# Performance work log

Measured on AMD Instinct MI355X. Metric: run time of the kernel, lower is better.

Reference implementation:

```python
import jax, jax.numpy as jnp
import numpy as np

B, N, D = 4, 2048, 1024
WIN, K, ALPHA = 4, 8, 0.3


def setup_inputs() -> dict:
    key = jax.random.key(0)
    ks = jax.random.split(key, 16)
    s_d = 1.0 / np.sqrt(D)
    s_2d = 1.0 / np.sqrt(2 * D)
    inp = {
        'mu': jax.random.normal(ks[0], (B, N, D), jnp.float32),
        'pheromone': jax.random.uniform(ks[1], (B, N), jnp.float32),
        'Wq': jax.random.normal(ks[2], (D, D), jnp.float32) * s_d,
        'bq': jnp.zeros((D,), jnp.float32),
        'Wk': jax.random.normal(ks[3], (D, D), jnp.float32) * s_d,
        'bk': jnp.zeros((D,), jnp.float32),
        'Wv': jax.random.normal(ks[4], (D, D), jnp.float32) * s_d,
        'bv': jnp.zeros((D,), jnp.float32),
        'Wm1': jax.random.normal(ks[5], (2 * D, D), jnp.float32) * s_2d,
        'bm1': jnp.zeros((D,), jnp.float32),
        'Wm2': jax.random.normal(ks[6], (D, D), jnp.float32) * s_d,
        'bm2': jnp.zeros((D,), jnp.float32),
        'Wo': jax.random.normal(ks[7], (2 * D, D), jnp.float32) * s_2d,
        'bo': jnp.zeros((D,), jnp.float32),
    }
    return inp


def reference(mu, pheromone, Wq, bq, Wk, bk, Wv, bv, Wm1, bm1, Wm2, bm2, Wo, bo):
    # ---- local windowed gather-MLP ----
    padded = jnp.pad(mu, ((0, 0), (WIN, 0), (0, 0)))  # causal left-pad
    neighbors = jnp.stack([padded[:, WIN - w:WIN - w + N, :] for w in range(1, WIN + 1)], axis=2)
    self_exp = jnp.broadcast_to(mu[:, :, None, :], neighbors.shape)
    cat = jnp.concatenate([self_exp, neighbors], axis=-1)
    h = jax.nn.silu(cat @ Wm1 + bm1) @ Wm2 + bm2
    local_msgs = h.mean(axis=2)  # (B,N,D)

    # ---- causal top-k attention with pheromone bias ----
    q = mu @ Wq + bq
    k = mu @ Wk + bk
    v = mu @ Wv + bv
    scale = 1.0 / jnp.sqrt(jnp.asarray(D, mu.dtype))
    scores = jnp.einsum('bnd,bmd->bnm', q, k) * scale  # (B,N,N)
    scores = scores + ALPHA * pheromone[:, None, :]
    row = jnp.arange(N)
    causal = jnp.where(row[None, :] > row[:, None], -jnp.inf, 0.0).astype(mu.dtype)
    scores = scores + causal[None]
    # top-k sparsification (N > K): softmax over the k kept scores, zeros elsewhere
    vals, idx = jax.lax.top_k(scores, K)  # (B,N,K)
    probs = jax.nn.softmax(vals, axis=-1)
    bi = jnp.arange(B)[:, None, None]
    ni = jnp.arange(N)[None, :, None]
    attn = jnp.zeros_like(scores).at[bi, ni, idx].set(probs)
    global_msgs = jnp.einsum('bnm,bmd->bnd', attn, v)

    return jnp.concatenate([local_msgs, global_msgs], axis=-1) @ Wo + bo
```

## Files before the change

### kernel.cpp

```cpp
#include <hip/hip_runtime.h>
#include <hip/hip_bf16.h>
#include <math.h>

#define B_ 4
#define N_ 2048
#define D_ 1024
#define WIN_ 4
#define KTOP 8
#define ALPHA_ 0.3f
#define SCALE_ (1.0f/32.0f)
#define NCH 16
#define INV2048 0.00048828125f

typedef unsigned short ushortT;
typedef _Float16 halfT;
typedef __attribute__((ext_vector_type(8))) _Float16 half8v;
typedef __attribute__((ext_vector_type(4))) float f32x4;

__device__ inline ushortT h2u(halfT h){ union{halfT h; ushortT u;} x; x.h=h; return x.u; }
__device__ inline halfT  u2h(ushortT u){ union{halfT h; ushortT u;} x; x.u=u; return x.h; }
__device__ inline float  uh2f(ushortT u){ return (float)u2h(u); }

__device__ __forceinline__ void gll16(const ushortT* g, ushortT* l) {
    __builtin_amdgcn_global_load_lds(
        (const __attribute__((address_space(1))) void*)g,
        (__attribute__((address_space(3))) void*)l, 16, 0, 0);
}

__global__ __launch_bounds__(256)
void prep_all(const float* __restrict__ mu, const float* __restrict__ Wm1,
              const float* __restrict__ Wm2, const float* __restrict__ Wv,
              const float* __restrict__ Wo, const float* __restrict__ Wq,
              const float* __restrict__ Wk,
              ushortT* __restrict__ mu_a, ushortT* __restrict__ mu_B,
              ushortT* __restrict__ WtF, ushortT* __restrict__ Wt_m2,
              ushortT* __restrict__ Wt_v, ushortT* __restrict__ Wt_o,
              ushortT* __restrict__ WqT_a, ushortT* __restrict__ WqT_B,
              ushortT* __restrict__ WkT_a, ushortT* __restrict__ WkT_B)
{
    const int bid = blockIdx.x;
    if (bid < 8192) {
        size_t base = ((size_t)bid * 256 + threadIdx.x) * 4;
        float4 v = *reinterpret_cast<const float4*>(&mu[base]);
        float vv[4] = {v.x, v.y, v.z, v.w};
        ushort4 pa, pb;
#pragma unroll
        for (int j = 0; j < 4; ++j) {
            float f = vv[j];
            halfT a = (halfT)f;  float r = f - (float)a;
            halfT b = (halfT)(r * 2048.0f);
            ((ushortT*)&pa)[j] = h2u(a); ((ushortT*)&pb)[j] = h2u(b);
        }
        *reinterpret_cast<ushort4*>(&mu_a[base]) = pa;
        *reinterpret_cast<ushort4*>(&mu_B[base]) = pb;
        return;
    }
    __shared__ float t[32][33];
    int b = bid - 8192;
    const float* W; ushortT* Pa; ushortT* Pb = nullptr;
    int K, lb, split = 0;
    if (b < 1024)      { W = Wm1;                       Pa = WtF;                     K = 1024; lb = b; }
    else if (b < 2048) { W = Wm1 + (size_t)1024 * 1024; Pa = WtF + (size_t)1024*1024; K = 1024; lb = b - 1024; }
    else if (b < 3072) { W = Wm2;  Pa = Wt_m2; K = 1024; lb = b - 2048; }
    else if (b < 4096) { W = Wv;   Pa = Wt_v;  K = 1024; lb = b - 3072; }
    else if (b < 6144) { W = Wo;   Pa = Wt_o;  K = 2048; lb = b - 4096; }
    else if (b < 7168) { W = Wq;   Pa = WqT_a; Pb = WqT_B; K = 1024; lb = b - 6144; split = 1; }
    else               { W = Wk;   Pa = WkT_a; Pb = WkT_B; K = 1024; lb = b - 7168; split = 1; }
    const int Nn = 1024;
    const int k0 = (K == 2048) ? (lb & 63) * 32 : (lb & 31) * 32;
    const int n0 = (K == 2048) ? (lb >> 6) * 32 : (lb >> 5) * 32;
    const int tx = threadIdx.x & 31, ty8 = threadIdx.x >> 5;
#pragma unroll
    for (int p = 0; p < 4; ++p) {
        int kk = p * 8 + ty8;
        t[kk][tx] = W[(size_t)(k0 + kk) * Nn + n0 + tx];
    }
    __syncthreads();
#pragma unroll
    for (int p = 0; p < 4; ++p) {
        int nn = p * 8 + ty8;
        float f = t[tx][nn];
        size_t o = (size_t)(n0 + nn) * K + k0 + tx;
        if (split) {
            halfT a = (halfT)f;  float r = f - (float)a;
            halfT bb = (halfT)(r * 2048.0f);
            Pa[o] = h2u(a); Pb[o] = h2u(bb);
        } else {
            Pa[o] = h2u((halfT)f);
        }
    }
}

__device__ __forceinline__ void gemm_core_h(
    const ushortT* __restrict__ A, int lda, const ushortT* __restrict__ Bt, int ldb,
    const float* __restrict__ bias, void* __restrict__ Cout, int ldc, int K,
    int m0, int n0, int outHalf, ushortT* AsL, ushortT* BsL)
{
    const int tid = threadIdx.x;
    const int w = tid >> 6, lane = tid & 63;
    const int wr = w >> 1, wc = w & 1;

    f32x4 acc[4][4];
#pragma unroll
    for (int mi = 0; mi < 4; ++mi)
#pragma unroll
        for (int ni = 0; ni < 4; ++ni) acc[mi][ni] = (f32x4){0.f, 0.f, 0.f, 0.f};

    for (int k0 = 0; k0 < K; k0 += 64) {
#pragma unroll
        for (int it = 0; it < 4; ++it) {
            int idx = tid + it * 256;
            int row = idx >> 3, c = idx & 7;
            int4 va = *reinterpret_cast<const int4*>(&A[(size_t)(m0 + row) * lda + k0 + c * 8]);
            *reinterpret_cast<int4*>(&AsL[row * 72 + c * 8]) = va;
            int4 vb = *reinterpret_cast<const int4*>(&Bt[(size_t)(n0 + row) * ldb + k0 + c * 8]);
            *reinterpret_cast<int4*>(&BsL[row * 72 + c * 8]) = vb;
        }
        __syncthreads();
#pragma unroll
        for (int kh = 0; kh < 2; ++kh) {
            const int ko = kh * 32 + (lane >> 4) * 8;
            const int rr = lane & 15;
            half8v af[4], bf[4];
#pragma unroll
            for (int mi = 0; mi < 4; ++mi)
                af[mi] = *reinterpret_cast<const half8v*>(&AsL[(wr * 64 + mi * 16 + rr) * 72 + ko]);
#pragma unroll
            for (int ni = 0; ni < 4; ++ni)
                bf[ni] = *reinterpret_cast<const half8v*>(&BsL[(wc * 64 + ni * 16 + rr) * 72 + ko]);
#pragma unroll
            for (int mi = 0; mi < 4; ++mi)
#pragma unroll
                for (int ni = 0; ni < 4; ++ni)
                    acc[mi][ni] = __builtin_amdgcn_mfma_f32_16x16x32_f16(
                        af[mi], bf[ni], acc[mi][ni], 0, 0, 0);
        }
        __syncthreads();
    }

    const int r4 = (lane >> 4) * 4, cl = lane & 15;
#pragma unroll
    for (int mi = 0; mi < 4; ++mi)
#pragma unroll
        for (int ni = 0; ni < 4; ++ni) {
            int row = m0 + wr * 64 + mi * 16 + r4;
            int col = n0 + wc * 64 + ni * 16 + cl;
            float bb = bias ? bias[col] : 0.f;
#pragma unroll
            for (int r = 0; r < 4; ++r) {
                float v = acc[mi][ni][r] + bb;
                if (outHalf)
                    ((ushortT*)Cout)[(size_t)(row + r) * ldc + col] = h2u((halfT)v);
                else
                    ((float*)Cout)[(size_t)(row + r) * ldc + col] = v;
            }
        }
}

template<int OUT_HALF>
__global__ __launch_bounds__(256)
void mfma_gemm_h(const ushortT* __restrict__ A, int lda,
                 const ushortT* __restrict__ Bt, int ldb,
                 const float* __restrict__ bias,
                 void* __restrict__ Cout, int ldc, int K)
{
    __shared__ ushortT AsL[128 * 72];
    __shared__ ushortT BsL[128 * 72];
    gemm_core_h(A, lda, Bt, ldb, bias, Cout, ldc, K,
                blockIdx.y * 128, blockIdx.x * 128, OUT_HALF, AsL, BsL);
}

__global__ __launch_bounds__(256)
void gemm_pf_v(const ushortT* __restrict__ mu_a,
               const ushortT* __restrict__ WtF, const ushortT* __restrict__ Wt_v,
               const float* __restrict__ bv,
               float* __restrict__ PF, ushortT* __restrict__ Vb16)
{
    __shared__ ushortT AsL[128 * 72];
    __shared__ ushortT BsL[128 * 72];
    const int bid = blockIdx.x;
    if (bid < 1024) {
        gemm_core_h(mu_a, D_, WtF, D_, (const float*)nullptr, (void*)PF, 2 * D_, D_,
                    (bid >> 4) * 128, (bid & 15) * 128, 0, AsL, BsL);
    } else {
        const int b2 = bid - 1024;
        gemm_core_h(mu_a, D_, Wt_v, D_, bv, (void*)Vb16, D_, D_,
                    (b2 >> 3) * 128, (b2 & 7) * 128, 1, AsL, BsL);
    }
}

__global__ __launch_bounds__(256)
void silu_mean(const float* __restrict__ P, const float* __restrict__ bm1,
               ushortT* __restrict__ Sb)
{
    size_t idx4 = (size_t)blockIdx.x * blockDim.x + threadIdx.x;
    size_t base = idx4 << 2;
    int row = (int)(base >> 10);
    int col = (int)(base & 1023);
    int n = row & (N_ - 1);
    float4 a = *reinterpret_cast<const float4*>(&P[(size_t)row * 2048 + col]);
    float4 bb = *reinterpret_cast<const float4*>(&bm1[col]);
    a.x += bb.x; a.y += bb.y; a.z += bb.z; a.w += bb.w;
    float sx = 0.f, sy = 0.f, sz = 0.f, sw = 0.f;
#pragma unroll
    for (int w = 1; w <= WIN_; ++w) {
        float xx = a.x, xy = a.y, xz = a.z, xw = a.w;
        if (n >= w) {
            const float4 nb = *reinterpret_cast<const float4*>(
                &P[(size_t)(row - w) * 2048 + 1024 + col]);
            xx += nb.x; xy += nb.y; xz += nb.z; xw += nb.w;
        }
        sx += xx / (1.f + __expf(-xx));
        sy += xy / (1.f + __expf(-xy));
        sz += xz / (1.f + __expf(-xz));
        sw += xw / (1.f + __expf(-xw));
    }
    ushort4 o = {h2u((halfT)(sx * 0.25f)), h2u((halfT)(sy * 0.25f)),
                 h2u((halfT)(sz * 0.25f)), h2u((halfT)(sw * 0.25f))};
    *reinterpret_cast<ushort4*>(&Sb[base]) = o;
}

__device__ inline void topk_insert(float (&tv)[KTOP], int (&ti)[KTOP], float s, int m)
{
    if ((s > tv[KTOP-1]) || (s == tv[KTOP-1] && m < ti[KTOP-1])) {
        float cs = s; int ci = m;
#pragma unroll
        for (int q = 0; q < KTOP; ++q) {
            bool beats = (cs > tv[q]) || (cs == tv[q] && ci < ti[q]);
            if (beats) { float t0 = tv[q]; int t1 = ti[q];
                         tv[q] = cs; ti[q] = ci; cs = t0; ci = t1; }
        }
    }
}

#define SPLIT3H_COMPUTE(Tb, wr, wc, lane, acc0, acc1)                           \
    {                                                                           \
        const int rr_ = (lane) & 15, q_ = (lane) >> 4;                          \
        const int Rb0_ = (wc) * 32 + rr_;                                       \
        const int Rb1_ = Rb0_ + 16;                                             \
        half8v ba0_ = *reinterpret_cast<const half8v*>(                         \
            &Tb[2 * 4096 + Rb0_ * 32 + ((q_ ^ ((Rb0_ >> 1) & 3)) << 3)]);       \
        half8v ba1_ = *reinterpret_cast<const half8v*>(                         \
            &Tb[2 * 4096 + Rb1_ * 32 + ((q_ ^ ((Rb1_ >> 1) & 3)) << 3)]);       \
        half8v bB0_ = *reinterpret_cast<const half8v*>(                         \
            &Tb[3 * 4096 + Rb0_ * 32 + ((q_ ^ ((Rb0_ >> 1) & 3)) << 3)]);       \
        half8v bB1_ = *reinterpret_cast<const half8v*>(                         \
            &Tb[3 * 4096 + Rb1_ * 32 + ((q_ ^ ((Rb1_ >> 1) & 3)) << 3)]);       \
        _Pragma("unroll")                                                       \
        for (int mi_ = 0; mi_ < 4; ++mi_) {                                     \
            const int Ra_ = (wr) * 64 + mi_ * 16 + rr_;                         \
            const int sw_ = (q_ ^ ((Ra_ >> 1) & 3)) << 3;                       \
            half8v aA_ = *reinterpret_cast<const half8v*>(&Tb[Ra_ * 32 + sw_]); \
            acc0[mi_][0] = __builtin_amdgcn_mfma_f32_16x16x32_f16(              \
                aA_, ba0_, acc0[mi_][0], 0, 0, 0);                              \
            acc0[mi_][1] = __builtin_amdgcn_mfma_f32_16x16x32_f16(              \
                aA_, ba1_, acc0[mi_][1], 0, 0, 0);                              \
            acc1[mi_][0] = __builtin_amdgcn_mfma_f32_16x16x32_f16(              \
                aA_, bB0_, acc1[mi_][0], 0, 0, 0);                              \
            acc1[mi_][1] = __builtin_amdgcn_mfma_f32_16x16x32_f16(              \
                aA_, bB1_, acc1[mi_][1], 0, 0, 0);                              \
        }                                                                       \
        _Pragma("unroll")                                                       \
        for (int mi_ = 0; mi_ < 4; ++mi_) {                                     \
            const int Ra_ = (wr) * 64 + mi_ * 16 + rr_;                         \
            const int sw_ = (q_ ^ ((Ra_ >> 1) & 3)) << 3;                       \
            half8v aB_ = *reinterpret_cast<const half8v*>(                      \
                &Tb[4096 + Ra_ * 32 + sw_]);                                    \
            acc1[mi_][0] = __builtin_amdgcn_mfma_f32_16x16x32_f16(              \
                aB_, ba0_, acc1[mi_][0], 0, 0, 0);                              \
            acc1[mi_][1] = __builtin_amdgcn_mfma_f32_16x16x32_f16(              \
                aB_, ba1_, acc1[mi_][1], 0, 0, 0);                              \
        }                                                                       \
    }

#define STAGE4(lb, koff)                                                        \
    {                                                                           \
        gll16(gp + goff + (koff), lb);                                          \
        gll16(gp + goff + (koff) + 16 * D_, (lb) + 512);                        \
        gll16(gp + goff + (koff) + 32 * D_, (lb) + 1024);                       \
        gll16(gp + goff + (koff) + 48 * D_, (lb) + 1536);                       \
    }

__global__ __launch_bounds__(512, 2)
void qk_proj(const ushortT* __restrict__ A0, const ushortT* __restrict__ A1,
             const ushortT* __restrict__ QWa, const ushortT* __restrict__ QWB,
             const ushortT* __restrict__ KWa, const ushortT* __restrict__ KWB,
             const float* __restrict__ bq, const float* __restrict__ bk,
             ushortT* __restrict__ Qa, ushortT* __restrict__ QB,
             ushortT* __restrict__ Ka, ushortT* __restrict__ KB)
{
    __shared__ ushortT TT[16384];

    const int half = blockIdx.x >> 9;
    int lin = blockIdx.x & 511;
    lin = (lin & 7) * 64 + (lin >> 3);
    const int m0 = (lin >> 3) * 128;
    const int n0 = (lin & 7) * 128;

    const ushortT* B0 = half ? KWa : QWa;
    const ushortT* B1 = half ? KWB : QWB;
    const float* bias = half ? bk : bq;
    ushortT* Pa = half ? Ka : Qa;
    ushortT* Pb = half ? KB : QB;

    const int tid = threadIdx.x;
    const int wid = tid >> 6, lane = tid & 63;
    const int wr = wid >> 2, wc = wid & 3;

    const int pl = wid >> 1;
    const int hb = (wid & 1) * 64;
    const ushortT* gp = (pl == 0) ? A0 : (pl == 1) ? A1 : (pl == 2) ? B0 : B1;
    const int rbase = (pl < 2 ? m0 : n0) + hb + (lane >> 2);
    const int cg8 = ((lane & 3) ^ ((lane >> 3) & 3)) << 3;
    const size_t goff = (size_t)rbase * D_ + cg8;
    ushortT* lb0 = &TT[pl * 4096 + hb * 32];

    f32x4 acc0[4][2], acc1[4][2];
#pragma unroll
    for (int mi = 0; mi < 4; ++mi) {
        acc0[mi][0] = (f32x4){0,0,0,0}; acc0[mi][1] = (f32x4){0,0,0,0};
        acc1[mi][0] = (f32x4){0,0,0,0}; acc1[mi][1] = (f32x4){0,0,0,0};
    }

    for (int ks = 0; ks < 32; ++ks) {
        STAGE4(lb0, (size_t)ks * 32)
        __syncthreads();
        __builtin_amdgcn_s_setprio(1);
        SPLIT3H_COMPUTE(TT, wr, wc, lane, acc0, acc1)
        __builtin_amdgcn_s_setprio(0);
        __syncthreads();
    }

    const int r4 = (lane >> 4) * 4, cl = lane & 15;
#pragma unroll
    for (int mi = 0; mi < 4; ++mi)
#pragma unroll
        for (int ni = 0; ni < 2; ++ni) {
            int col = n0 + wc * 32 + ni * 16 + cl;
            float bb = bias[col];
#pragma unroll
            for (int r = 0; r < 4; ++r) {
                int row = m0 + wr * 64 + mi * 16 + r4 + r;
                float v = acc0[mi][ni][r] + INV2048 * acc1[mi][ni][r] + bb;
                halfT a = (halfT)v;  float r1 = v - (float)a;
                halfT b = (halfT)(r1 * 2048.0f);
                size_t o = (size_t)row * D_ + col;
                Pa[o] = h2u(a); Pb[o] = h2u(b);
            }
        }
}

__global__ __launch_bounds__(512, 2)
void attn_scores_h(const ushortT* __restrict__ Qa, const ushortT* __restrict__ QB,
                   const ushortT* __restrict__ Ka, const ushortT* __restrict__ KB,
                   const float* __restrict__ pher,
                   float* __restrict__ WV, int* __restrict__ WI)
{
    __shared__ ushortT TT[16384];
    __shared__ float Ps[128];
    __shared__ float PV[32 * 4 * 8];
    __shared__ int   PI[32 * 4 * 8];
    float* MV = reinterpret_cast<float*>(&TT[0]);
    int*   MI = reinterpret_cast<int*>((char*)&TT[0] + 16384);

    int lin = blockIdx.y * 136 + blockIdx.x;
    lin = (lin & 7) * 68 + (lin >> 3);
    const int b = lin / 136;
    const int xy = lin - b * 136;
    int g = 0;
    while ((g + 1) * (g + 2) / 2 <= xy) ++g;
    const int ch = xy - g * (g + 1) / 2;
    const int n0 = g * 128;
    const int m0 = ch * 128;
    const size_t bN = (size_t)b * N_;

    const int tid = threadIdx.x;
    const int wid = tid >> 6, lane = tid & 63;
    const int wr = wid >> 2, wc = wid & 3;

    if (tid < 128) Ps[tid] = pher[bN + m0 + tid];

    const int pl = wid >> 1;
    const int hb = (wid & 1) * 64;
    const ushortT* gp = (pl == 0) ? Qa : (pl == 1) ? QB : (pl == 2) ? Ka : KB;
    const size_t rbase = bN + (pl < 2 ? n0 : m0) + hb + (lane >> 2);
    const int cg8 = ((lane & 3) ^ ((lane >> 3) & 3)) << 3;
    const size_t goff = rbase * (size_t)D_ + cg8;
    ushortT* lb0 = &TT[pl * 4096 + hb * 32];

    f32x4 acc0[4][2], acc1[4][2];
#pragma unroll
    for (int mi = 0; mi < 4; ++mi) {
        acc0[mi][0] = (f32x4){0,0,0,0}; acc0[mi][1] = (f32x4){0,0,0,0};
        acc1[mi][0] = (f32x4){0,0,0,0}; acc1[mi][1] = (f32x4){0,0,0,0};
    }

    for (int ks = 0; ks < 32; ++ks) {
        STAGE4(lb0, (size_t)ks * 32)
        __syncthreads();
        __builtin_amdgcn_s_setprio(1);
        SPLIT3H_COMPUTE(TT, wr, wc, lane, acc0, acc1)
        __builtin_amdgcn_s_setprio(0);
        __syncthreads();
    }

    const int r4 = (lane >> 4) * 4, cl = lane & 15;
    for (int p = 0; p < 4; ++p) {
        __syncthreads();
        if (wr == (p >> 1)) {
#pragma unroll
            for (int mi2 = 0; mi2 < 2; ++mi2) {
                const int mi = (p & 1) * 2 + mi2;
#pragma unroll
                for (int ni = 0; ni < 2; ++ni) {
                    int col = wc * 32 + ni * 16 + cl;
                    int m = m0 + col;
#pragma unroll
                    for (int r = 0; r < 4; ++r) {
                        int rloc = mi2 * 16 + r4 + r;
                        int n = n0 + p * 32 + rloc;
                        bool ok = (m <= n);
                        float sc = acc0[mi][ni][r] + INV2048 * acc1[mi][ni][r];
                        MV[rloc * 128 + col] = ok ? (sc * SCALE_ + ALPHA_ * Ps[col])
                                                  : -INFINITY;
                        MI[rloc * 128 + col] = ok ? m : 0x7fffffff;
                    }
                }
            }
        }
        __syncthreads();
        if (tid < 128) {
            const int row = tid >> 2, q4 = tid & 3;
            float tv[KTOP]; int ti[KTOP];
#pragma unroll
            for (int j = 0; j < KTOP; ++j) { tv[j] = -INFINITY; ti[j] = 0x7fffffff; }
            for (int j = 0; j < 32; ++j) {
                float s2 = MV[row * 128 + q4 * 32 + j];
                if (s2 == -INFINITY) continue;
                topk_insert(tv, ti, s2, MI[row * 128 + q4 * 32 + j]);
            }
#pragma unroll
            for (int j = 0; j < KTOP; ++j) {
                PV[(row * 4 + q4) * 8 + j] = tv[j];
                PI[(row * 4 + q4) * 8 + j] = ti[j];
            }
        }
        __syncthreads();
        if (tid < 32) {
            float tv[KTOP]; int ti[KTOP];
#pragma unroll
            for (int j = 0; j < KTOP; ++j) { tv[j] = -INFINITY; ti[j] = 0x7fffffff; }
            for (int i = 0; i < 32; ++i) {
                float s2 = PV[tid * 32 + i];
                if (s2 == -INFINITY) continue;
                topk_insert(tv, ti, s2, PI[tid * 32 + i]);
            }
            int n = n0 + p * 32 + tid;
            size_t base = ((bN + n) * NCH + ch) * 8;
#pragma unroll
            for (int j = 0; j < KTOP; ++j) { WV[base + j] = tv[j]; WI[base + j] = ti[j]; }
        }
    }
}

__global__ __launch_bounds__(256)
void attn_merge(const float* __restrict__ WV, const int* __restrict__ WI,
                const ushortT* __restrict__ V, ushortT* __restrict__ CCb)
{
    __shared__ float CV[4][128];
    __shared__ int   CI[4][128];
    __shared__ float Pp[4][KTOP];
    __shared__ int   Pi[4][KTOP];

    const int tid  = threadIdx.x;
    const int wv   = tid >> 6;
    const int lane = tid & 63;
    const int rid  = blockIdx.x * 4 + wv;
    const int b    = rid >> 11;
    const int n    = rid & (N_ - 1);
    const int ncand = ((n >> 7) + 1) * 8;
    const size_t cbase = (size_t)rid * (NCH * 8);

#pragma unroll
    for (int t = 0; t < 2; ++t) {
        int i = lane + t * 64;
        if (i < ncand) { CV[wv][i] = WV[cbase + i]; CI[wv][i] = WI[cbase + i]; }
        else           { CV[wv][i] = -INFINITY;     CI[wv][i] = 0x7fffffff;   }
    }
    __syncthreads();

    if (lane == 0) {
        float tv[KTOP]; int ti[KTOP];
#pragma unroll
        for (int j = 0; j < KTOP; ++j) { tv[j] = -INFINITY; ti[j] = 0x7fffffff; }
        for (int i = 0; i < 128; ++i) {
            float s = CV[wv][i];
            if (s == -INFINITY) continue;
            topk_insert(tv, ti, s, CI[wv][i]);
        }
        float mx = tv[0];
        float e[KTOP]; float sum = 0.f;
#pragma unroll
        for (int j = 0; j < KTOP; ++j) {
            e[j] = (tv[j] == -INFINITY) ? 0.f : __expf(tv[j] - mx);
            sum += e[j];
        }
        float inv = 1.f / sum;
#pragma unroll
        for (int j = 0; j < KTOP; ++j) {
            Pp[wv][j] = e[j] * inv;
            Pi[wv][j] = (tv[j] == -INFINITY) ? 0 : ti[j];
        }
    }
    __syncthreads();

    const size_t vbase = (size_t)b * N_ * D_;
#pragma unroll
    for (int it = 0; it < 2; ++it) {
        int c8 = (it * 64 + lane) * 8;
        float o[8];
#pragma unroll
        for (int u = 0; u < 8; ++u) o[u] = 0.f;
#pragma unroll
        for (int j = 0; j < KTOP; ++j) {
            float p = Pp[wv][j];
            ushort4 v0 = *reinterpret_cast<const ushort4*>(
                &V[vbase + (size_t)Pi[wv][j] * D_ + c8]);
            ushort4 v1 = *reinterpret_cast<const ushort4*>(
                &V[vbase + (size_t)Pi[wv][j] * D_ + c8 + 4]);
            o[0] = fmaf(p, uh2f(v0.x), o[0]); o[1] = fmaf(p, uh2f(v0.y), o[1]);
            o[2] = fmaf(p, uh2f(v0.z), o[2]); o[3] = fmaf(p, uh2f(v0.w), o[3]);
            o[4] = fmaf(p, uh2f(v1.x), o[4]); o[5] = fmaf(p, uh2f(v1.y), o[5]);
            o[6] = fmaf(p, uh2f(v1.z), o[6]); o[7] = fmaf(p, uh2f(v1.w), o[7]);
        }
        ushort4 ob0 = {h2u((halfT)o[0]), h2u((halfT)o[1]), h2u((halfT)o[2]), h2u((halfT)o[3])};
        ushort4 ob1 = {h2u((halfT)o[4]), h2u((halfT)o[5]), h2u((halfT)o[6]), h2u((halfT)o[7])};
        *reinterpret_cast<ushort4*>(&CCb[(size_t)rid * 2048 + 1024 + c8]) = ob0;
        *reinterpret_cast<ushort4*>(&CCb[(size_t)rid * 2048 + 1024 + c8 + 4]) = ob1;
    }
}

extern "C" void kernel_launch(void* const* d_in, const int* in_sizes, int n_in,
                              void* d_out, int out_size, void* d_ws, size_t ws_size,
                              hipStream_t stream)
{
    const float* mu   = (const float*)d_in[0];
    const float* pher = (const float*)d_in[1];
    const float* Wq   = (const float*)d_in[2];
    const float* bq   = (const float*)d_in[3];
    const float* Wk   = (const float*)d_in[4];
    const float* bk   = (const float*)d_in[5];
    const float* Wv   = (const float*)d_in[6];
    const float* bv   = (const float*)d_in[7];
    const float* Wm1  = (const float*)d_in[8];
    const float* bm1  = (const float*)d_in[9];
    const float* Wm2  = (const float*)d_in[10];
    const float* bm2  = (const float*)d_in[11];
    const float* Wo   = (const float*)d_in[12];
    const float* bo   = (const float*)d_in[13];
    float* out = (float*)d_out;
    float* ws  = (float*)d_ws;

    const size_t SZ  = (size_t)B_ * N_ * D_;
    const size_t MEG = 1024 * 1024;
    const int M = B_ * N_;

    ushortT* CCb  = (ushortT*)ws;
    float*   PF   = ws + SZ;
    ushortT* Qa   = (ushortT*)(ws + SZ);
    ushortT* QB   = Qa + SZ;
    ushortT* Ka   = (ushortT*)(ws + 2 * SZ);
    ushortT* KB   = Ka + SZ;
    ushortT* mu_a = (ushortT*)(ws + 3 * SZ);
    ushortT* mu_B = mu_a + SZ;
    ushortT* Sb   = (ushortT*)(ws + 4 * SZ);
    float*   WVb  = (float*)(ws + 4 * SZ);
    int*     WIb  = (int*)(WVb + MEG);
    ushortT* Vb16 = (ushortT*)(ws + 4 * SZ + 4 * MEG);
    ushortT* U    = (ushortT*)(ws + 4 * SZ + 8 * MEG);
    ushortT* WtF  = U;
    ushortT* Wt_m2 = U + 2 * MEG;
    ushortT* Wt_v  = U + 3 * MEG;
    ushortT* WqT_a = U + 4 * MEG;        ushortT* WqT_B = U + 5 * MEG;
    ushortT* WkT_a = U + 6 * MEG;        ushortT* WkT_B = U + 7 * MEG;
    ushortT* Wt_o  = U + 8 * MEG;

    dim3 blk256(256), blk512(512);
    dim3 gD(8, 64);

    hipLaunchKernelGGL(prep_all, dim3(16384), blk256, 0, stream,
                       mu, Wm1, Wm2, Wv, Wo, Wq, Wk,
                       mu_a, mu_B, WtF, Wt_m2, Wt_v, Wt_o,
                       WqT_a, WqT_B, WkT_a, WkT_B);
    hipLaunchKernelGGL(gemm_pf_v, dim3(1536), blk256, 0, stream,
                       mu_a, WtF, Wt_v, bv, PF, Vb16);
    hipLaunchKernelGGL(silu_mean, dim3(SZ / 4 / 256), blk256, 0, stream, PF, bm1, Sb);
    hipLaunchKernelGGL((mfma_gemm_h<1>), gD, blk256, 0, stream,
                       Sb, D_, Wt_m2, D_, bm2, (void*)CCb, 2 * D_, D_);
    hipLaunchKernelGGL(qk_proj, dim3(1024), blk512, 0, stream,
                       mu_a, mu_B, WqT_a, WqT_B, WkT_a, WkT_B,
                       bq, bk, Qa, QB, Ka, KB);
    hipLaunchKernelGGL(attn_scores_h, dim3(136, B_), blk512, 0, stream,
                       Qa, QB, Ka, KB, pher, WVb, WIb);
    hipLaunchKernelGGL(attn_merge, dim3(M / 4), blk256, 0, stream, WVb, WIb, Vb16, CCb);
    hipLaunchKernelGGL((mfma_gemm_h<0>), gD, blk256, 0, stream,
                       CCb, 2 * D_, Wt_o, 2048, bo, (void*)out, D_, 2 * D_);

    (void)in_sizes; (void)n_in; (void)out_size; (void)ws_size;
}
```

Measured before the change: 739.7 us.

## Merge Wm2 GEMM into QK projection launch as extra independent blocks

```diff
diff --git a/kernel.cpp b/kernel.cpp
--- a/kernel.cpp
+++ b/kernel.cpp
@@ -282,15 +282,81 @@
     }
 
 __global__ __launch_bounds__(512, 2)
-void qk_proj(const ushortT* __restrict__ A0, const ushortT* __restrict__ A1,
+void mid_all(const ushortT* __restrict__ A0, const ushortT* __restrict__ A1,
              const ushortT* __restrict__ QWa, const ushortT* __restrict__ QWB,
              const ushortT* __restrict__ KWa, const ushortT* __restrict__ KWB,
              const float* __restrict__ bq, const float* __restrict__ bk,
              ushortT* __restrict__ Qa, ushortT* __restrict__ QB,
-             ushortT* __restrict__ Ka, ushortT* __restrict__ KB)
-{
-    __shared__ ushortT TT[16384];
-
+             ushortT* __restrict__ Ka, ushortT* __restrict__ KB,
+             const ushortT* __restrict__ Sb, const ushortT* __restrict__ Wt_m2,
+             const float* __restrict__ bm2, ushortT* __restrict__ CCb)
+{
+    __shared__ ushortT SMEM[18432];
+
+    const int tid = threadIdx.x;
+    const int wid = tid >> 6, lane = tid & 63;
+
+    if (blockIdx.x >= 1024) {
+        const int t = blockIdx.x - 1024;
+        const int m0 = (t >> 3) * 128;
+        const int n0 = (t & 7) * 128;
+        ushortT* AsL = SMEM;
+        ushortT* BsL = SMEM + 9216;
+        const int wr = wid >> 2, wc = wid & 3;
+
+        f32x4 acc[4][2];
+#pragma unroll
+        for (int mi = 0; mi < 4; ++mi) { acc[mi][0] = (f32x4){0,0,0,0}; acc[mi][1] = (f32x4){0,0,0,0}; }
+
+        for (int k0 = 0; k0 < D_; k0 += 64) {
+#pragma unroll
+            for (int it = 0; it < 2; ++it) {
+                int idx = tid + it * 512;
+                int row = idx >> 3, c = idx & 7;
+                int4 va = *reinterpret_cast<const int4*>(&Sb[(size_t)(m0 + row) * D_ + k0 + c * 8]);
+                *reinterpret_cast<int4*>(&AsL[row * 72 + c * 8]) = va;
+                int4 vb = *reinterpret_cast<const int4*>(&Wt_m2[(size_t)(n0 + row) * D_ + k0 + c * 8]);
+                *reinterpret_cast<int4*>(&BsL[row * 72 + c * 8]) = vb;
+            }
+            __syncthreads();
+#pragma unroll
+            for (int kh = 0; kh < 2; ++kh) {
+                const int ko = kh * 32 + (lane >> 4) * 8;
+                const int rr = lane & 15;
+                half8v af[4], bf[2];
+#pragma unroll
+                for (int mi = 0; mi < 4; ++mi)
+                    af[mi] = *reinterpret_cast<const half8v*>(&AsL[(wr * 64 + mi * 16 + rr) * 72 + ko]);
+#pragma unroll
+                for (int ni = 0; ni < 2; ++ni)
+                    bf[ni] = *reinterpret_cast<const half8v*>(&BsL[(wc * 32 + ni * 16 + rr) * 72 + ko]);
+#pragma unroll
+                for (int mi = 0; mi < 4; ++mi)
+#pragma unroll
+                    for (int ni = 0; ni < 2; ++ni)
+                        acc[mi][ni] = __builtin_amdgcn_mfma_f32_16x16x32_f16(
+                            af[mi], bf[ni], acc[mi][ni], 0, 0, 0);
+            }
+            __syncthreads();
+        }
+
+        const int r4 = (lane >> 4) * 4, cl = lane & 15;
+#pragma unroll
+        for (int mi = 0; mi < 4; ++mi)
+#pragma unroll
+            for (int ni = 0; ni < 2; ++ni) {
+                int col = n0 + wc * 32 + ni * 16 + cl;
+                float bb = bm2[col];
+#pragma unroll
+                for (int r = 0; r < 4; ++r) {
+                    int row = m0 + wr * 64 + mi * 16 + r4 + r;
+                    CCb[(size_t)row * 2048 + col] = h2u((halfT)(acc[mi][ni][r] + bb));
+                }
+            }
+        return;
+    }
+
+    ushortT* TT = SMEM;
     const int half = blockIdx.x >> 9;
     int lin = blockIdx.x & 511;
     lin = (lin & 7) * 64 + (lin >> 3);
@@ -303,10 +369,7 @@
     ushortT* Pa = half ? Ka : Qa;
     ushortT* Pb = half ? KB : QB;
 
-    const int tid = threadIdx.x;
-    const int wid = tid >> 6, lane = tid & 63;
     const int wr = wid >> 2, wc = wid & 3;
-
     const int pl = wid >> 1;
     const int hb = (wid & 1) * 64;
     const ushortT* gp = (pl == 0) ? A0 : (pl == 1) ? A1 : (pl == 2) ? B0 : B1;
@@ -595,11 +658,10 @@
     hipLaunchKernelGGL(gemm_pf_v, dim3(1536), blk256, 0, stream,
                        mu_a, WtF, Wt_v, bv, PF, Vb16);
     hipLaunchKernelGGL(silu_mean, dim3(SZ / 4 / 256), blk256, 0, stream, PF, bm1, Sb);
-    hipLaunchKernelGGL((mfma_gemm_h<1>), gD, blk256, 0, stream,
-                       Sb, D_, Wt_m2, D_, bm2, (void*)CCb, 2 * D_, D_);
-    hipLaunchKernelGGL(qk_proj, dim3(1024), blk512, 0, stream,
+    hipLaunchKernelGGL(mid_all, dim3(1536), blk512, 0, stream,
                        mu_a, mu_B, WqT_a, WqT_B, WkT_a, WkT_B,
-                       bq, bk, Qa, QB, Ka, KB);
+                       bq, bk, Qa, QB, Ka, KB,
+                       Sb, Wt_m2, bm2, CCb);
     hipLaunchKernelGGL(attn_scores_h, dim3(136, B_), blk512, 0, stream,
                        Qa, QB, Ka, KB, pher, WVb, WIb);
     hipLaunchKernelGGL(attn_merge, dim3(M / 4), blk256, 0, stream, WVb, WIb, Vb16, CCb);
```

Measured after the change: 739.1 us. Within noise of the previous version (-0.1%).
